# Kernel tuning notes

Measured on AMD Instinct MI355X. Metric: run time of the kernel, lower is better.

The kernel has to match this reference:

```python
import jax, jax.numpy as jnp
import numpy as np

B, S, D = 2, 2048, 2048
H, HD = 16, 128
ROPE_THETA = 10000.0


def _rope_cos_sin(seq_len, head_dim, dtype=jnp.float32):
    inv_freq = 1.0 / (ROPE_THETA ** (jnp.arange(0, head_dim, 2, dtype=jnp.float32) / head_dim))
    t = jnp.arange(seq_len, dtype=jnp.float32)
    freqs = jnp.outer(t, inv_freq)                     # [S, HD/2]
    emb = jnp.concatenate([freqs, freqs], axis=-1)     # [S, HD]
    return jnp.cos(emb).astype(dtype), jnp.sin(emb).astype(dtype)


def _rotate_half(x):
    x1, x2 = jnp.split(x, 2, axis=-1)
    return jnp.concatenate([-x2, x1], axis=-1)


def _apply_rope(x, cos, sin):
    # x: [B, S, H, HD]; cos/sin: [S, HD] -> broadcast over batch and heads
    c = cos[None, :, None, :]
    s = sin[None, :, None, :]
    return x * c + _rotate_half(x) * s


def setup_inputs() -> dict:
    key = jax.random.key(0)
    ks = jax.random.split(key, 6)
    scale = 1.0 / np.sqrt(D)
    hidden_states = jax.random.normal(ks[0], (B, S, D), dtype=jnp.float32)
    # causal additive mask: 0 on/below diagonal, large negative above
    neg = jnp.finfo(jnp.float32).min
    causal = jnp.where(jnp.tril(jnp.ones((S, S), dtype=bool)), 0.0, neg)
    attention_mask = jnp.broadcast_to(causal[None, None, :, :], (B, 1, S, S)).astype(jnp.float32)
    Wq = jax.random.normal(ks[1], (D, D), dtype=jnp.float32) * scale
    Wk = jax.random.normal(ks[2], (D, D), dtype=jnp.float32) * scale
    Wv = jax.random.normal(ks[3], (D, D), dtype=jnp.float32) * scale
    Wo = jax.random.normal(ks[4], (D, D), dtype=jnp.float32) * scale
    return {"hidden_states": hidden_states, "attention_mask": attention_mask,
            "Wq": Wq, "Wk": Wk, "Wv": Wv, "Wo": Wo}


def reference(hidden_states, attention_mask, Wq, Wk, Wv, Wo):
    b, s, d = hidden_states.shape
    # projections (torch Linear: x @ W^T)
    q = (hidden_states @ Wq.T).reshape(b, s, H, HD)
    k = (hidden_states @ Wk.T).reshape(b, s, H, HD)
    v = (hidden_states @ Wv.T).reshape(b, s, H, HD)
    cos, sin = _rope_cos_sin(s, HD, hidden_states.dtype)
    q = _apply_rope(q, cos, sin)
    k = _apply_rope(k, cos, sin)
    # naive attention, [B, H, S, S] scores materialized as in the original
    scores = jnp.einsum('bqhd,bkhd->bhqk', q, k) / np.sqrt(HD)
    scores = scores + attention_mask
    attn = jax.nn.softmax(scores, axis=-1)
    out = jnp.einsum('bhqk,bkhd->bqhd', attn, v).reshape(b, s, d)
    return out @ Wo.T
```

## Files before the change

kernel.cpp:

```cpp
#include <hip/hip_runtime.h>
#include <hip/hip_bf16.h>

typedef __hip_bfloat16 bf16;
typedef __attribute__((ext_vector_type(8))) short s16x8;
typedef __attribute__((ext_vector_type(4))) float f32x4;
typedef __attribute__((ext_vector_type(16))) float f32x16;

#define MFMA16(a, b, c) __builtin_amdgcn_mfma_f32_16x16x32_bf16(a, b, c, 0, 0, 0)
#define MFMA32(a, b, c) __builtin_amdgcn_mfma_f32_32x32x16_bf16(a, b, c, 0, 0, 0)

#define GLL16(gsrc, ldst)                                                                 \
  __builtin_amdgcn_global_load_lds(                                                       \
      (const __attribute__((address_space(1))) unsigned int*)(gsrc),                      \
      (__attribute__((address_space(3))) unsigned int*)(ldst), 16, 0, 0)

#define VMCNT(n) asm volatile("s_waitcnt vmcnt(" #n ")" ::: "memory")
#define BARRIER() __builtin_amdgcn_s_barrier()

static constexpr int S_LEN = 2048;
static constexpr int D_DIM = 2048;
static constexpr int NY = 6144;

union BF4 { ushort4 u; bf16 b[4]; };

__device__ inline unsigned pack2(float a, float b) {
  union { bf16 h[2]; unsigned u; } x;
  x.h[0] = __float2bfloat16(a);
  x.h[1] = __float2bfloat16(b);
  return x.u;
}

__global__ void convert_all(const float* __restrict__ X, const float* __restrict__ Wq,
                            const float* __restrict__ Wk, const float* __restrict__ Wv,
                            const float* __restrict__ Wo, bf16* __restrict__ Xb,
                            bf16* __restrict__ Wb, bf16* __restrict__ Wob,
                            float* __restrict__ cosT, float* __restrict__ sinT) {
  int gid = blockIdx.x * 256 + threadIdx.x;
  if (gid < 6291456) {
    int i4 = gid * 4;
    const float* src;
    bf16* dst;
    int off;
    if (i4 < 8388608) {
      src = X; dst = Xb; off = i4;
    } else {
      int j = i4 - 8388608;
      int seg = j >> 22;
      off = j & 4194303;
      if (seg == 0) { src = Wq; dst = Wb; }
      else if (seg == 1) { src = Wk; dst = Wb + 4194304; }
      else if (seg == 2) { src = Wv; dst = Wb + 8388608; }
      else { src = Wo; dst = Wob; }
    }
    float4 v = *(const float4*)(src + off);
    BF4 o;
    o.b[0] = __float2bfloat16(v.x);
    o.b[1] = __float2bfloat16(v.y);
    o.b[2] = __float2bfloat16(v.z);
    o.b[3] = __float2bfloat16(v.w);
    *(ushort4*)(dst + off) = o.u;
  } else {
    int t4 = (gid - 6291456) * 4;
    if (t4 < 131072) {
#pragma unroll
      for (int k = 0; k < 4; ++k) {
        int i = t4 + k;
        int d = i & 63, s = i >> 6;
        float inv = powf(10000.0f, -(float)d * (1.0f / 64.0f));
        float ang = (float)s * inv;
        cosT[i] = cosf(ang);
        sinT[i] = sinf(ang);
      }
    }
  }
}

__global__ __launch_bounds__(256) void rope_tv(bf16* __restrict__ Y,
                                               const float* __restrict__ cosT,
                                               const float* __restrict__ sinT,
                                               bf16* __restrict__ Vt) {
  __shared__ bf16 tile[32][36];
  const int bid = blockIdx.x;
  const int t = threadIdx.x;
  if (bid < 8192) {
    int idx = bid * 256 + t;
    int quad = idx & 15;
    int h = (idx >> 4) & 15;
    int m = (idx >> 8) & 4095;
    int g = idx >> 20;
    int s = m & (S_LEN - 1);
    int d0 = quad * 4;
    float sc = g ? 1.0f : 0.08838834764831845f;
    bf16* p = Y + (size_t)m * NY + g * D_DIM + h * 128 + d0;
    BF4 lo, hi, olo, ohi;
    lo.u = *(const ushort4*)p;
    hi.u = *(const ushort4*)(p + 64);
    float4 c = *(const float4*)(cosT + s * 64 + d0);
    float4 sn = *(const float4*)(sinT + s * 64 + d0);
    float cc[4] = {c.x, c.y, c.z, c.w};
    float ss[4] = {sn.x, sn.y, sn.z, sn.w};
#pragma unroll
    for (int i = 0; i < 4; ++i) {
      float x1 = __bfloat162float(lo.b[i]);
      float x2 = __bfloat162float(hi.b[i]);
      olo.b[i] = __float2bfloat16((x1 * cc[i] - x2 * ss[i]) * sc);
      ohi.b[i] = __float2bfloat16((x2 * cc[i] + x1 * ss[i]) * sc);
    }
    *(ushort4*)p = olo.u;
    *(ushort4*)(p + 64) = ohi.u;
  } else {
    int id = bid - 8192;
    int bx = id & 63, by = (id >> 6) & 3, bh = id >> 8;
    int b = bh >> 4, h = bh & 15;
    int s0 = bx * 32, d0 = by * 32;
    int r = t >> 3;
    int c4 = (t & 7) * 4;
    BF4 in;
    in.u = *(const ushort4*)(Y + (size_t)(b * S_LEN + s0 + r) * NY + 4096 + h * 128 + d0 + c4);
    *(ushort4*)(&tile[r][c4]) = in.u;
    __syncthreads();
    BF4 o;
#pragma unroll
    for (int i = 0; i < 4; ++i) o.b[i] = tile[c4 + i][r];
    *(ushort4*)(Vt + (size_t)bh * 128 * S_LEN + (size_t)(d0 + r) * S_LEN + s0 + c4) = o.u;
  }
}

__device__ inline void storeC(float* p, float v) { *p = v; }
__device__ inline void storeC(bf16* p, float v) { *p = __float2bfloat16(v); }

template <typename OutT>
__global__ __launch_bounds__(512, 2) void gemm_fine(const bf16* __restrict__ A,
                                                    const bf16* __restrict__ Bm,
                                                    OutT* __restrict__ C, int K, int lda,
                                                    int ldb, int ldc, int mt) {
  __shared__ __align__(16) char lds[147456];
  char* b0 = lds;
  char* b1 = lds + 49152;
  char* b2 = lds + 98304;
  const int tid = threadIdx.x;
  const int lane = tid & 63;
  const int w = tid >> 6;
  const int wm = w >> 2, wn = w & 3;
  const int l15 = lane & 15, lh4 = lane >> 4;
  const int xr = l15 & 7;
  const int xo0 = ((lh4 ^ xr) << 4);
  const int xo1 = (((4 + lh4) ^ xr) << 4);

  const int nwg = gridDim.x;
  const int bid = blockIdx.x;
  const int swz = (bid & 7) * (nwg >> 3) + (bid >> 3);
  const int bm = swz % mt, bn = swz / mt;
  const int row0 = bm * 128, col0 = bn * 256;

  const int srow = w * 8 + (lane >> 3);
  const int scol = ((lane & 7) ^ (lane >> 3)) * 8;
  const bf16* gA = A + (size_t)(row0 + srow) * lda + scol;
  const bf16* gB = Bm + (size_t)(col0 + srow) * ldb + scol;
  const int ldst = w * 1024;

  f32x4 acc[4][4];
#pragma unroll
  for (int i = 0; i < 4; ++i)
#pragma unroll
    for (int j = 0; j < 4; ++j) acc[i][j] = (f32x4){0.f, 0.f, 0.f, 0.f};

  s16x8 af[4], bfr[4];

#define PH_READ(BUF, XO)                                                          \
  _Pragma("unroll") for (int ii = 0; ii < 4; ++ii)                                \
      af[ii] = *(const s16x8*)((BUF) + (wm * 64 + ii * 16 + l15) * 128 + (XO));   \
  _Pragma("unroll") for (int jj = 0; jj < 4; ++jj)                                \
      bfr[jj] = *(const s16x8*)((BUF) + 16384 + (wn * 64 + jj * 16 + l15) * 128 + (XO));
#define PH_FMA()                                                                  \
  __builtin_amdgcn_s_setprio(1);                                                  \
  _Pragma("unroll") for (int jj = 0; jj < 4; ++jj)                                \
  _Pragma("unroll") for (int ii = 0; ii < 4; ++ii)                                \
      acc[ii][jj] = MFMA16(af[ii], bfr[jj], acc[ii][jj]);                         \
  __builtin_amdgcn_s_setprio(0);
#define STAGE_T(BUF, kS)                                                          \
  GLL16(gA + (kS), (BUF) + ldst);                                                 \
  GLL16(gA + (size_t)64 * lda + (kS), (BUF) + 8192 + ldst);                       \
  GLL16(gB + (kS), (BUF) + 16384 + ldst);                                         \
  GLL16(gB + (size_t)64 * ldb + (kS), (BUF) + 24576 + ldst);                      \
  GLL16(gB + (size_t)128 * ldb + (kS), (BUF) + 32768 + ldst);                     \
  GLL16(gB + (size_t)192 * ldb + (kS), (BUF) + 40960 + ldst);
#define TILE_MAIN(RBUF, SBUF, kS)                                                 \
  PH_READ(RBUF, xo0);                                                             \
  GLL16(gA + (kS), (SBUF) + ldst);                                                \
  GLL16(gA + (size_t)64 * lda + (kS), (SBUF) + 8192 + ldst);                      \
  GLL16(gB + (kS), (SBUF) + 16384 + ldst);                                        \
  BARRIER();                                                                      \
  PH_FMA();                                                                       \
  BARRIER();                                                                      \
  PH_READ(RBUF, xo1);                                                             \
  GLL16(gB + (size_t)64 * ldb + (kS), (SBUF) + 24576 + ldst);                     \
  GLL16(gB + (size_t)128 * ldb + (kS), (SBUF) + 32768 + ldst);                    \
  GLL16(gB + (size_t)192 * ldb + (kS), (SBUF) + 40960 + ldst);                    \
  BARRIER();                                                                      \
  PH_FMA();                                                                       \
  VMCNT(6);                                                                       \
  BARRIER();

  STAGE_T(b0, 0);
  STAGE_T(b1, 64);
  VMCNT(6);
  BARRIER();

  const int NT = K >> 6;
  for (int t = 0; t < NT - 2; t += 3) {
    TILE_MAIN(b0, b2, (size_t)(t + 2) * 64);
    TILE_MAIN(b1, b0, (size_t)(t + 3) * 64);
    TILE_MAIN(b2, b1, (size_t)(t + 4) * 64);
  }
  PH_READ(b0, xo0);
  BARRIER();
  PH_FMA();
  BARRIER();
  PH_READ(b0, xo1);
  BARRIER();
  PH_FMA();
  VMCNT(0);
  BARRIER();
  PH_READ(b1, xo0);
  BARRIER();
  PH_FMA();
  BARRIER();
  PH_READ(b1, xo1);
  BARRIER();
  PH_FMA();
#undef PH_READ
#undef PH_FMA
#undef STAGE_T
#undef TILE_MAIN

#pragma unroll
  for (int mi = 0; mi < 4; ++mi)
#pragma unroll
    for (int ni = 0; ni < 4; ++ni) {
      int gr = row0 + wm * 64 + mi * 16 + lh4 * 4;
      int gc = col0 + wn * 64 + ni * 16 + l15;
#pragma unroll
      for (int rr = 0; rr < 4; ++rr)
        storeC(&C[(size_t)(gr + rr) * ldc + gc], acc[mi][ni][rr]);
    }
}

__global__ __launch_bounds__(256, 2) void attn_fwd(const bf16* __restrict__ Y,
                                                   const bf16* __restrict__ Vt,
                                                   bf16* __restrict__ At) {
  __shared__ __align__(16) char smem[32768];
  bf16* Ks = (bf16*)smem;
  bf16* Vs = (bf16*)(smem + 16384);

  const int idx = blockIdx.x;
  const int qt = 15 - (idx >> 5);
  const int bh = idx & 31;
  const int b = bh >> 4, h = bh & 15;
  const int tid = threadIdx.x;
  const int lane = tid & 63;
  const int w = tid >> 6;
  const int l31 = lane & 31;
  const int hi = lane >> 5;
  const int q0w = qt * 128 + w * 32;
  const int q = q0w + l31;

  s16x8 qf[8];
  {
    const bf16* qb = Y + (size_t)(b * S_LEN + q) * NY + h * 128 + hi * 8;
#pragma unroll
    for (int s = 0; s < 8; ++s) qf[s] = *(const s16x8*)(qb + s * 16);
  }

  f32x16 O[4];
#pragma unroll
  for (int d = 0; d < 4; ++d)
#pragma unroll
    for (int e = 0; e < 16; ++e) O[d][e] = 0.f;
  float m_run = -3.0e38f, l_run = 0.f;

  const bf16* Kbase = Y + (size_t)(b * S_LEN) * NY + 2048 + h * 128;
  const bf16* Vbase = Vt + (size_t)bh * 128 * S_LEN;
  const int tmax = 2 * qt + 1;

  for (int t = 0; t <= tmax; ++t) {
    const int kv0 = t * 64;
    __syncthreads();
#pragma unroll
    for (int j = 0; j < 4; ++j) {
      int rk = j * 16 + w * 4 + (lane >> 4);
      int ck = lane & 15;
      GLL16(Kbase + (size_t)(kv0 + rk) * NY + ((ck ^ (rk & 15)) * 8),
            Ks + (j * 2048 + w * 512));
      int dv = j * 32 + w * 8 + (lane >> 3);
      int cv = lane & 7;
      GLL16(Vbase + (size_t)dv * S_LEN + kv0 + ((cv ^ (dv & 7)) * 8),
            Vs + (j * 2048 + w * 512));
    }
    __syncthreads();
    if (kv0 > q0w + 31) continue;

    float sv[32];
#pragma unroll
    for (int tt = 0; tt < 2; ++tt) {
      f32x16 sa;
#pragma unroll
      for (int e = 0; e < 16; ++e) sa[e] = 0.f;
      const int rk = tt * 32 + l31;
      const char* kr = (const char*)Ks + rk * 256;
      const int xr = (rk & 15) << 4;
#pragma unroll
      for (int s = 0; s < 8; ++s) {
        s16x8 kf = *(const s16x8*)(kr + ((s * 32 + hi * 16) ^ xr));
        sa = MFMA32(kf, qf[s], sa);
      }
#pragma unroll
      for (int e = 0; e < 16; ++e) sv[tt * 16 + e] = sa[e];
    }

    if (kv0 + 63 > q0w) {
#pragma unroll
      for (int tt = 0; tt < 2; ++tt)
#pragma unroll
        for (int r = 0; r < 16; ++r) {
          int kvr = kv0 + tt * 32 + (r & 3) + 8 * (r >> 2) + 4 * hi;
          if (kvr > q) sv[tt * 16 + r] = -3.0e38f;
        }
    }

    float mx[16];
#pragma unroll
    for (int i = 0; i < 16; ++i) mx[i] = fmaxf(sv[i], sv[i + 16]);
#pragma unroll
    for (int st = 8; st >= 1; st >>= 1)
#pragma unroll
      for (int i = 0; i < 8; ++i)
        if (i < st) mx[i] = fmaxf(mx[i], mx[i + st]);
    float pmax = fmaxf(mx[0], __shfl_xor(mx[0], 32, 64));

    bool need = pmax > m_run + 8.0f;
    if (__any(need)) {
      float newm = fmaxf(m_run, pmax);
      float ef = __expf(m_run - newm);
      m_run = newm;
      l_run *= ef;
#pragma unroll
      for (int d = 0; d < 4; ++d)
#pragma unroll
        for (int e = 0; e < 16; ++e) O[d][e] *= ef;
    }

    float rsum = 0.f;
#pragma unroll
    for (int i = 0; i < 32; ++i) {
      sv[i] = __expf(sv[i] - m_run);
      rsum += sv[i];
    }
    rsum += __shfl_xor(rsum, 32, 64);
    l_run += rsum;

    unsigned pw[4][4];
#pragma unroll
    for (int tt = 0; tt < 2; ++tt) {
      const int bs = tt * 16;
      unsigned x01 = pack2(sv[bs + 0], sv[bs + 1]);
      unsigned x23 = pack2(sv[bs + 2], sv[bs + 3]);
      unsigned x45 = pack2(sv[bs + 4], sv[bs + 5]);
      unsigned x67 = pack2(sv[bs + 6], sv[bs + 7]);
      unsigned y01 = pack2(sv[bs + 8], sv[bs + 9]);
      unsigned y23 = pack2(sv[bs + 10], sv[bs + 11]);
      unsigned y45 = pack2(sv[bs + 12], sv[bs + 13]);
      unsigned y67 = pack2(sv[bs + 14], sv[bs + 15]);
      unsigned sx01 = __shfl_xor(x01, 32, 64), sx23 = __shfl_xor(x23, 32, 64);
      unsigned sx45 = __shfl_xor(x45, 32, 64), sx67 = __shfl_xor(x67, 32, 64);
      unsigned sy01 = __shfl_xor(y01, 32, 64), sy23 = __shfl_xor(y23, 32, 64);
      unsigned sy45 = __shfl_xor(y45, 32, 64), sy67 = __shfl_xor(y67, 32, 64);
      pw[tt * 2][0] = hi ? sx45 : x01;
      pw[tt * 2][1] = hi ? sx67 : x23;
      pw[tt * 2][2] = hi ? x45 : sx01;
      pw[tt * 2][3] = hi ? x67 : sx23;
      pw[tt * 2 + 1][0] = hi ? sy45 : y01;
      pw[tt * 2 + 1][1] = hi ? sy67 : y23;
      pw[tt * 2 + 1][2] = hi ? y45 : sy01;
      pw[tt * 2 + 1][3] = hi ? y67 : sy23;
    }

#pragma unroll
    for (int dt = 0; dt < 4; ++dt) {
      const int d = dt * 32 + l31;
      const char* vr = (const char*)Vs + d * 128;
      const int xv = (d & 7) << 4;
#pragma unroll
      for (int sl = 0; sl < 4; ++sl) {
        s16x8 vf = *(const s16x8*)(vr + ((sl * 32 + hi * 16) ^ xv));
        union { unsigned u[4]; s16x8 v; } pb;
        pb.u[0] = pw[sl][0];
        pb.u[1] = pw[sl][1];
        pb.u[2] = pw[sl][2];
        pb.u[3] = pw[sl][3];
        O[dt] = MFMA32(vf, pb.v, O[dt]);
      }
    }
  }

  __syncthreads();
  const float inv = 1.0f / l_run;
  {
    const int orow = w * 32 + l31;
    const int xo = (orow & 15) << 4;
    char* obase = (char*)smem + orow * 256;
#pragma unroll
    for (int dt = 0; dt < 4; ++dt)
#pragma unroll
      for (int r = 0; r < 16; ++r) {
        int d = dt * 32 + (r & 3) + 8 * (r >> 2) + 4 * hi;
        *(bf16*)(obase + ((d * 2) ^ xo)) = __float2bfloat16(O[dt][r] * inv);
      }
  }
  __syncthreads();
  bf16* dst = At + (size_t)(b * S_LEN + qt * 128) * D_DIM + h * 128;
#pragma unroll
  for (int j = 0; j < 8; ++j) {
    int id = j * 256 + tid;
    int rr = id >> 4, cc = id & 15;
    int4 val = *(const int4*)((char*)smem + rr * 256 + ((cc * 16) ^ ((rr & 15) << 4)));
    *(int4*)(dst + (size_t)rr * D_DIM + cc * 8) = val;
  }
}

extern "C" void kernel_launch(void* const* d_in, const int* in_sizes, int n_in,
                              void* d_out, int out_size, void* d_ws, size_t ws_size,
                              hipStream_t stream) {
  const float* X = (const float*)d_in[0];
  const float* Wq = (const float*)d_in[2];
  const float* Wk = (const float*)d_in[3];
  const float* Wv = (const float*)d_in[4];
  const float* Wo = (const float*)d_in[5];
  float* out = (float*)d_out;
  char* ws = (char*)d_ws;

  bf16* Xb = (bf16*)(ws);
  bf16* Wb = (bf16*)(ws + 16777216);
  bf16* Wob = (bf16*)(ws + 41943040);
  bf16* Y = (bf16*)(ws + 50331648);
  bf16* Vt = (bf16*)(ws + 100663296);
  bf16* At = (bf16*)(ws + 117440512);
  float* cosT = (float*)(ws + 134217728);
  float* sinT = (float*)(ws + 134742016);

  convert_all<<<24704, 256, 0, stream>>>(X, Wq, Wk, Wv, Wo, Xb, Wb, Wob, cosT, sinT);

  gemm_fine<bf16><<<768, 512, 0, stream>>>(Xb, Wb, Y, 2048, 2048, 2048, 6144, 32);
  rope_tv<<<16384, 256, 0, stream>>>(Y, cosT, sinT, Vt);
  attn_fwd<<<512, 256, 0, stream>>>(Y, Vt, At);
  gemm_fine<float><<<256, 512, 0, stream>>>(At, Wob, out, 2048, 2048, 2048, 2048, 32);
}
```

Measured before the change: 257.2 us.

## Double-buffer K/V tiles in attention with async prefetch of next tile

Doubles attention LDS to two 32KB K/V buffers. The next KV tile's global-to-LDS loads are issued before computing the current one, with a partial vmcnt wait in place of the full sync. This hides global load latency behind the MFMA work. It raises LDS per block to 64KB, which may limit occupancy at two blocks per CU, and the vmcnt accounting must match exactly the eight loads issued per stage.

```diff
diff --git a/kernel.cpp b/kernel.cpp
--- a/kernel.cpp
+++ b/kernel.cpp
@@ -249,9 +249,7 @@
 __global__ __launch_bounds__(256, 2) void attn_fwd(const bf16* __restrict__ Y,
                                                    const bf16* __restrict__ Vt,
                                                    bf16* __restrict__ At) {
-  __shared__ __align__(16) char smem[32768];
-  bf16* Ks = (bf16*)smem;
-  bf16* Vs = (bf16*)(smem + 16384);
+  __shared__ __align__(16) char smem[65536];
 
   const int idx = blockIdx.x;
   const int qt = 15 - (idx >> 5);
@@ -283,21 +281,37 @@
   const bf16* Vbase = Vt + (size_t)bh * 128 * S_LEN;
   const int tmax = 2 * qt + 1;
 
+  const int rk_ = w * 4 + (lane >> 4);
+  const int ck_ = lane & 15;
+  const int dv_ = w * 8 + (lane >> 3);
+  const int cv_ = lane & 7;
+
+#define STAGE_KV(T, BASE)                                                         \
+  {                                                                               \
+    const int kv0s = (T)*64;                                                      \
+    _Pragma("unroll") for (int j = 0; j < 4; ++j) {                               \
+      int rk = j * 16 + rk_;                                                      \
+      GLL16(Kbase + (size_t)(kv0s + rk) * NY + ((ck_ ^ (rk & 15)) * 8),           \
+            (BASE) + (j * 4096 + w * 1024));                                      \
+      int dv = j * 32 + dv_;                                                      \
+      GLL16(Vbase + (size_t)dv * S_LEN + kv0s + ((cv_ ^ (dv & 7)) * 8),           \
+            (BASE) + 16384 + (j * 4096 + w * 1024));                              \
+    }                                                                             \
+  }
+
+  STAGE_KV(0, smem);
+
   for (int t = 0; t <= tmax; ++t) {
     const int kv0 = t * 64;
-    __syncthreads();
-#pragma unroll
-    for (int j = 0; j < 4; ++j) {
-      int rk = j * 16 + w * 4 + (lane >> 4);
-      int ck = lane & 15;
-      GLL16(Kbase + (size_t)(kv0 + rk) * NY + ((ck ^ (rk & 15)) * 8),
-            Ks + (j * 2048 + w * 512));
-      int dv = j * 32 + w * 8 + (lane >> 3);
-      int cv = lane & 7;
-      GLL16(Vbase + (size_t)dv * S_LEN + kv0 + ((cv ^ (dv & 7)) * 8),
-            Vs + (j * 2048 + w * 512));
-    }
-    __syncthreads();
+    const char* cur = smem + (t & 1) * 32768;
+    BARRIER();
+    if (t < tmax) {
+      STAGE_KV(t + 1, smem + ((t + 1) & 1) * 32768);
+      VMCNT(8);
+    } else {
+      VMCNT(0);
+    }
+    BARRIER();
     if (kv0 > q0w + 31) continue;
 
     float sv[32];
@@ -307,7 +321,7 @@
 #pragma unroll
       for (int e = 0; e < 16; ++e) sa[e] = 0.f;
       const int rk = tt * 32 + l31;
-      const char* kr = (const char*)Ks + rk * 256;
+      const char* kr = cur + rk * 256;
       const int xr = (rk & 15) << 4;
 #pragma unroll
       for (int s = 0; s < 8; ++s) {
@@ -388,7 +402,7 @@
 #pragma unroll
     for (int dt = 0; dt < 4; ++dt) {
       const int d = dt * 32 + l31;
-      const char* vr = (const char*)Vs + d * 128;
+      const char* vr = cur + 16384 + d * 128;
       const int xv = (d & 7) << 4;
 #pragma unroll
       for (int sl = 0; sl < 4; ++sl) {
@@ -402,6 +416,7 @@
       }
     }
   }
+#undef STAGE_KV
 
   __syncthreads();
   const float inv = 1.0f / l_run;
```

Result: no change. 253.5 us (-1.4%).
